# Kernel optimization log

Hardware: AMD Instinct MI355X
Metric: run time of the kernel (lower is better)

## Reference

```python
import jax, jax.numpy as jnp
import numpy as np

B, S, E = 2, 2048, 4096
H, KVH, D = 32, 8, 128
GROUPS = H // KVH
MAX_POS = 4096
ROPE_THETA = 10000.0


def _rope_tables(max_pos, dim, theta):
    inv_freq = 1.0 / (theta ** (jnp.arange(0, dim, 2, dtype=jnp.float32) / dim))
    t = jnp.arange(max_pos, dtype=jnp.float32)
    freqs = jnp.einsum('i,j->ij', t, inv_freq)        # [max_pos, dim/2]
    emb = jnp.concatenate([freqs, freqs], axis=-1)    # [max_pos, dim]
    return jnp.cos(emb), jnp.sin(emb)


def _rotate_half(x):
    x1, x2 = x[..., : x.shape[-1] // 2], x[..., x.shape[-1] // 2:]
    return jnp.concatenate([-x2, x1], axis=-1)


def setup_inputs() -> dict:
    key = jax.random.key(0)
    ks = jax.random.split(key, 8)
    scale_w = 1.0 / np.sqrt(E)
    query = jax.random.normal(ks[0], (B, S, E), dtype=jnp.float32)
    k_in = jax.random.normal(ks[1], (B, S, E), dtype=jnp.float32)
    v_in = jax.random.normal(ks[2], (B, S, E), dtype=jnp.float32)
    position_ids = jnp.broadcast_to(jnp.arange(S, dtype=jnp.int64), (B, S))
    # causal mask: 1 where attending allowed, 0 elsewhere
    src_mask = jnp.tril(jnp.ones((S, S), dtype=jnp.int32))
    src_mask = jnp.broadcast_to(src_mask, (B, S, S))
    Wq = jax.random.normal(ks[3], (E, H * D), dtype=jnp.float32) * scale_w
    Wk = jax.random.normal(ks[4], (E, KVH * D), dtype=jnp.float32) * scale_w
    Wv = jax.random.normal(ks[5], (E, KVH * D), dtype=jnp.float32) * scale_w
    Wo = jax.random.normal(ks[6], (H * D, E), dtype=jnp.float32) * scale_w
    return {"query": query, "key": k_in, "value": v_in,
            "position_ids": position_ids, "src_mask": src_mask,
            "Wq": Wq, "Wk": Wk, "Wv": Wv, "Wo": Wo}


def reference(query, key, value, position_ids, src_mask, Wq, Wk, Wv, Wo):
    nb, q_len, _ = query.shape
    # projections -> [B, heads, S, D]
    q = (query @ Wq).reshape(nb, q_len, H, D).transpose(0, 2, 1, 3)
    k = (key @ Wk).reshape(nb, q_len, KVH, D).transpose(0, 2, 1, 3)
    v = (value @ Wv).reshape(nb, q_len, KVH, D).transpose(0, 2, 1, 3)
    # RoPE
    cos_t, sin_t = _rope_tables(MAX_POS, D, ROPE_THETA)
    cos = cos_t[position_ids][:, None]  # [B,1,S,D]
    sin = sin_t[position_ids][:, None]
    q = q * cos + _rotate_half(q) * sin
    k = k * cos + _rotate_half(k) * sin
    # repeat_kv (interleave groups) -> [B,H,S,D]
    k = jnp.repeat(k, GROUPS, axis=1)
    v = jnp.repeat(v, GROUPS, axis=1)
    # attention core
    scores = jnp.einsum('bhqd,bhkd->bhqk', q, k) / jnp.sqrt(jnp.float32(D))
    mask = src_mask[:, None]  # [B,1,S,S]
    scores = jnp.where(mask == 0, jnp.float32(-1e9), scores)
    attn = jax.nn.softmax(scores, axis=-1)
    x = jnp.einsum('bhqk,bhkd->bhqd', attn, v)
    x = x.transpose(0, 2, 1, 3).reshape(nb, q_len, H * D)
    return x @ Wo
```

## Files before the change

kernel.cpp:

```cpp
#include <hip/hip_runtime.h>
#include <stdint.h>

#define B_ 2
#define S_ 2048
#define E_ 4096
#define H_ 32
#define KVH_ 8
#define D_ 128

typedef __bf16 bf16_t;
typedef __bf16 bf16x8 __attribute__((ext_vector_type(8)));
typedef __bf16 bf16x4 __attribute__((ext_vector_type(4)));
typedef float f32x4 __attribute__((ext_vector_type(4)));

__device__ __forceinline__ void gl2lds16(const void* g, void* l) {
  __builtin_amdgcn_global_load_lds(
      (__attribute__((address_space(1))) void*)(uintptr_t)g,
      (__attribute__((address_space(3))) void*)(uint32_t)(uintptr_t)l,
      16, 0, 0);
}

__global__ void cvt_f32_bf16(const float* __restrict__ in, bf16_t* __restrict__ out, int n4) {
  int i = blockIdx.x * 256 + threadIdx.x;
  if (i < n4) {
    float4 v = ((const float4*)in)[i];
    bf16x4 o;
    o.x = (bf16_t)v.x; o.y = (bf16_t)v.y; o.z = (bf16_t)v.z; o.w = (bf16_t)v.w;
    ((bf16x4*)out)[i] = o;
  }
}

__global__ void transpose_cvt(const float* __restrict__ in, bf16_t* __restrict__ out,
                              int R, int C) {
  __shared__ float t[32][33];
  int r0 = blockIdx.y * 32, c0 = blockIdx.x * 32;
  int tx = threadIdx.x & 31, tg = threadIdx.x >> 5;
#pragma unroll
  for (int k = 0; k < 4; ++k) {
    int r = tg * 4 + k;
    t[r][tx] = in[(long)(r0 + r) * C + c0 + tx];
  }
  __syncthreads();
#pragma unroll
  for (int k = 0; k < 4; ++k) {
    int r = tg * 4 + k;
    out[(long)(c0 + r) * R + r0 + tx] = (bf16_t)t[tx][r];
  }
}

__global__ void transpose_v(const float* __restrict__ Vtmp, bf16_t* __restrict__ Vt) {
  __shared__ float t[32][33];
  int z = blockIdx.z, b = z >> 3, kv = z & 7;
  const float* in = Vtmp + (long)b * S_ * (KVH_ * D_) + kv * D_;
  bf16_t* out = Vt + ((long)(b * KVH_ + kv)) * D_ * S_;
  int s0 = blockIdx.y * 32, d0 = blockIdx.x * 32;
  int tx = threadIdx.x & 31, tg = threadIdx.x >> 5;
#pragma unroll
  for (int k = 0; k < 4; ++k) {
    int r = tg * 4 + k;
    t[r][tx] = in[(long)(s0 + r) * (KVH_ * D_) + d0 + tx];
  }
  __syncthreads();
#pragma unroll
  for (int k = 0; k < 4; ++k) {
    int r = tg * 4 + k;
    out[(long)(d0 + r) * S_ + s0 + tx] = (bf16_t)t[tx][r];
  }
}

__global__ void rope_cvt(const float* __restrict__ T, bf16_t* __restrict__ out,
                         const int* __restrict__ pos, int NH, float scale) {
  long idx = (long)blockIdx.x * 256 + threadIdx.x;
  int j = (int)(idx & 63);
  long t = idx >> 6;
  int s = (int)(t % S_); t /= S_;
  int nh = (int)(t % NH);
  int b = (int)(t / NH);
  long row = ((long)b * S_ + s) * ((long)NH * D_) + (long)nh * D_;
  float x1 = T[row + j];
  float x2 = T[row + j + 64];
  float p = (float)pos[(long)b * S_ + s];
  float inv = expf(-(float)j * (9.210340371976184f / 64.0f));
  float fr = p * inv;
  float c = cosf(fr), sn = sinf(fr);
  long ob = (((long)b * NH + nh) * S_ + s) * D_;
  out[ob + j]      = (bf16_t)((x1 * c - x2 * sn) * scale);
  out[ob + j + 64] = (bf16_t)((x2 * c + x1 * sn) * scale);
}

__global__ __launch_bounds__(256, 2) void gemm_bt(
    const bf16_t* __restrict__ A, const bf16_t* __restrict__ Bt,
    float* __restrict__ C, int M, int N, int K) {
  __shared__ bf16_t As[128 * 64];
  __shared__ bf16_t Bs[128 * 64];
  const int tid = threadIdx.x;
  const int lane = tid & 63;
  const int wave = tid >> 6;
  const int m0 = blockIdx.y * 128, n0 = blockIdx.x * 128;
  const int wm = (wave >> 1) * 64, wn = (wave & 1) * 64;
  const int ln = lane & 15, quad = lane >> 4;
  const int srow = lane >> 3;
  const int sg = lane & 7;

  f32x4 acc[4][4] = {};

  for (int kb = 0; kb < K; kb += 64) {
    __syncthreads();
#pragma unroll
    for (int it = 0; it < 4; ++it) {
      int c = wave * 4 + it;
      int row = c * 8 + srow;
      int g = sg ^ (row & 7);
      gl2lds16(A + (long)(m0 + row) * K + kb + g * 8, &As[c * 512 + lane * 8]);
      gl2lds16(Bt + (long)(n0 + row) * K + kb + g * 8, &Bs[c * 512 + lane * 8]);
    }
    __syncthreads();
#pragma unroll
    for (int ks = 0; ks < 2; ++ks) {
      bf16x8 af[4], bfr[4];
      const int go = ((ks * 4 + quad) ^ (ln & 7)) * 8;
#pragma unroll
      for (int i = 0; i < 4; ++i)
        af[i] = *(const bf16x8*)&As[(wm + i * 16 + ln) * 64 + go];
#pragma unroll
      for (int j = 0; j < 4; ++j)
        bfr[j] = *(const bf16x8*)&Bs[(wn + j * 16 + ln) * 64 + go];
#pragma unroll
      for (int i = 0; i < 4; ++i)
#pragma unroll
        for (int j = 0; j < 4; ++j)
          acc[i][j] = __builtin_amdgcn_mfma_f32_16x16x32_bf16(af[i], bfr[j], acc[i][j], 0, 0, 0);
    }
  }
#pragma unroll
  for (int i = 0; i < 4; ++i)
#pragma unroll
    for (int j = 0; j < 4; ++j)
#pragma unroll
      for (int r = 0; r < 4; ++r) {
        int m = m0 + wm + i * 16 + quad * 4 + r;
        int n = n0 + wn + j * 16 + ln;
        C[(long)m * N + n] = acc[i][j][r];
      }
}

#define QBLK_ 256
#define KVBLK_ 64
__global__ __launch_bounds__(512, 1) void flash_attn(
    const bf16_t* __restrict__ Q, const bf16_t* __restrict__ Kr,
    const bf16_t* __restrict__ Vt, bf16_t* __restrict__ X) {
  __shared__ bf16_t Ks[3][KVBLK_ * D_];
  __shared__ bf16_t Vs[3][D_ * KVBLK_];
  __shared__ bf16_t Plds[8][32 * KVBLK_];
  const int tid = threadIdx.x, lane = tid & 63, wave = tid >> 6;
  const int ln = lane & 15, quad = lane >> 4;

  const int d = blockIdx.x;
  const int wid = (d & 7) * 64 + (d >> 3);
  const int qb = 7 - (wid & 7);
  const int h = (wid >> 3) & 31;
  const int b = wid >> 8;
  const int kv = h >> 2;
  const bf16_t* Kbase = Kr + (((long)b * KVH_ + kv) * S_) * D_;
  const bf16_t* Vbase = Vt + (((long)b * KVH_ + kv) * D_) * S_;
  bf16_t* Pw = Plds[wave];

  const int nt = 4 * qb + 4;
  const int jlast = 4 * qb + (wave >> 1);

  bf16x8 aq[2][4];
  {
    const bf16_t* Qw = Q + (((long)b * H_ + h) * S_ + qb * QBLK_ + wave * 32) * D_;
#pragma unroll
    for (int i = 0; i < 2; ++i)
#pragma unroll
      for (int ks = 0; ks < 4; ++ks)
        aq[i][ks] = *(const bf16x8*)(Qw + (i * 16 + ln) * D_ + ks * 32 + quad * 8);
  }
  asm volatile("s_waitcnt vmcnt(0)" ::: "memory");

  auto STAGE = [&](int bi, int jt) {
    const bf16_t* Kt = Kbase + (long)jt * KVBLK_ * D_;
    const int vcol = jt * KVBLK_;
#pragma unroll
    for (int it = 0; it < 2; ++it) {
      int c = wave * 2 + it;
      int krow = c * 4 + quad;
      int kg = ln ^ (krow & 15);
      gl2lds16(Kt + krow * D_ + kg * 8, &Ks[bi][c * 512 + lane * 8]);
      int vrow = c * 8 + (lane >> 3);
      int vg = (lane & 7) ^ (vrow & 7);
      gl2lds16(Vbase + (long)vrow * S_ + vcol + vg * 8, &Vs[bi][c * 512 + lane * 8]);
    }
  };

  f32x4 o_acc[2][8] = {};
  float m_cur[2][4], l_par[2][4];
#pragma unroll
  for (int i = 0; i < 2; ++i)
#pragma unroll
    for (int r = 0; r < 4; ++r) { m_cur[i][r] = -__builtin_inff(); l_par[i][r] = 0.f; }

  STAGE(0, 0);
  STAGE(1, 1);

  for (int jt = 0; jt < nt; ++jt) {
    if (jt < nt - 1) asm volatile("s_waitcnt vmcnt(4)" ::: "memory");
    else             asm volatile("s_waitcnt vmcnt(0)" ::: "memory");
    __builtin_amdgcn_s_barrier();
    __builtin_amdgcn_sched_barrier(0);
    if (jt + 2 < nt) STAGE((jt + 2) % 3, jt + 2);

    if (jt <= jlast) {
      const bf16_t* Kb = Ks[jt % 3];
      const bf16_t* Vb = Vs[jt % 3];

      f32x4 s_acc[2][4] = {};
#pragma unroll
      for (int ks = 0; ks < 4; ++ks) {
        bf16x8 bk[4];
        const int go = ((ks * 4 + quad) ^ ln) * 8;
#pragma unroll
        for (int j = 0; j < 4; ++j)
          bk[j] = *(const bf16x8*)&Kb[(j * 16 + ln) * D_ + go];
        __builtin_amdgcn_s_setprio(1);
#pragma unroll
        for (int i = 0; i < 2; ++i)
#pragma unroll
          for (int j = 0; j < 4; ++j)
            s_acc[i][j] = __builtin_amdgcn_mfma_f32_16x16x32_bf16(aq[i][ks], bk[j], s_acc[i][j], 0, 0, 0);
        __builtin_amdgcn_s_setprio(0);
      }

#pragma unroll
      for (int i = 0; i < 2; ++i) {
        float rmax[4];
#pragma unroll
        for (int r = 0; r < 4; ++r) rmax[r] = -__builtin_inff();
#pragma unroll
        for (int j = 0; j < 4; ++j)
#pragma unroll
          for (int r = 0; r < 4; ++r) {
            float v = s_acc[i][j][r];
            if (jt == jlast) {
              int qrow = qb * QBLK_ + wave * 32 + i * 16 + quad * 4 + r;
              int kcol = jt * KVBLK_ + j * 16 + ln;
              if (kcol > qrow) v = -__builtin_inff();
            }
            s_acc[i][j][r] = v;
            rmax[r] = fmaxf(rmax[r], v);
          }
#pragma unroll
        for (int r = 0; r < 4; ++r) {
          float v = rmax[r];
          v = fmaxf(v, __shfl_xor(v, 1));
          v = fmaxf(v, __shfl_xor(v, 2));
          v = fmaxf(v, __shfl_xor(v, 4));
          v = fmaxf(v, __shfl_xor(v, 8));
          rmax[r] = v;
        }
        float grow = fmaxf(fmaxf(rmax[0] - m_cur[i][0], rmax[1] - m_cur[i][1]),
                           fmaxf(rmax[2] - m_cur[i][2], rmax[3] - m_cur[i][3]));
        if (__any(grow > 8.0f)) {
          float alpha[4];
#pragma unroll
          for (int r = 0; r < 4; ++r) {
            float mn = fmaxf(m_cur[i][r], rmax[r]);
            alpha[r] = exp2f(m_cur[i][r] - mn);
            m_cur[i][r] = mn;
            l_par[i][r] *= alpha[r];
          }
#pragma unroll
          for (int j = 0; j < 8; ++j)
#pragma unroll
            for (int r = 0; r < 4; ++r)
              o_acc[i][j][r] *= alpha[r];
        }
#pragma unroll
        for (int j = 0; j < 4; ++j)
#pragma unroll
          for (int r = 0; r < 4; ++r) {
            float p = exp2f(s_acc[i][j][r] - m_cur[i][r]);
            s_acc[i][j][r] = p;
            l_par[i][r] += p;
          }
#pragma unroll
        for (int j = 0; j < 4; ++j)
#pragma unroll
          for (int r = 0; r < 4; ++r) {
            int prow = i * 16 + quad * 4 + r;
            int pg = (j * 2 + (ln >> 3)) ^ (prow & 7);
            Pw[prow * KVBLK_ + pg * 8 + (ln & 7)] = (bf16_t)s_acc[i][j][r];
          }
      }

#pragma unroll
      for (int ks = 0; ks < 2; ++ks) {
        bf16x8 ap[2], bv[8];
        const int go = ((ks * 4 + quad) ^ (ln & 7)) * 8;
#pragma unroll
        for (int i = 0; i < 2; ++i)
          ap[i] = *(const bf16x8*)&Pw[(i * 16 + ln) * KVBLK_ + go];
#pragma unroll
        for (int j = 0; j < 8; ++j)
          bv[j] = *(const bf16x8*)&Vb[(j * 16 + ln) * KVBLK_ + go];
        __builtin_amdgcn_s_setprio(1);
#pragma unroll
        for (int i = 0; i < 2; ++i)
#pragma unroll
          for (int j = 0; j < 8; ++j)
            o_acc[i][j] = __builtin_amdgcn_mfma_f32_16x16x32_bf16(ap[i], bv[j], o_acc[i][j], 0, 0, 0);
        __builtin_amdgcn_s_setprio(0);
      }
    }
  }

#pragma unroll
  for (int i = 0; i < 2; ++i) {
    float rl[4];
#pragma unroll
    for (int r = 0; r < 4; ++r) {
      float lsum = l_par[i][r];
      lsum += __shfl_xor(lsum, 1);
      lsum += __shfl_xor(lsum, 2);
      lsum += __shfl_xor(lsum, 4);
      lsum += __shfl_xor(lsum, 8);
      rl[r] = 1.0f / lsum;
    }
#pragma unroll
    for (int j = 0; j < 8; ++j)
#pragma unroll
      for (int r = 0; r < 4; ++r) {
        int q = qb * QBLK_ + wave * 32 + i * 16 + quad * 4 + r;
        int dcol = j * 16 + ln;
        float o = o_acc[i][j][r] * rl[r];
        X[((long)b * S_ + q) * (H_ * D_) + (long)h * D_ + dcol] = (bf16_t)o;
      }
  }
}

extern "C" void kernel_launch(void* const* d_in, const int* in_sizes, int n_in,
                              void* d_out, int out_size, void* d_ws, size_t ws_size,
                              hipStream_t stream) {
  const float* query = (const float*)d_in[0];
  const float* key   = (const float*)d_in[1];
  const float* value = (const float*)d_in[2];
  const int*   pos   = (const int*)d_in[3];
  const float* Wq = (const float*)d_in[5];
  const float* Wk = (const float*)d_in[6];
  const float* Wv = (const float*)d_in[7];
  const float* Wo = (const float*)d_in[8];
  float* out = (float*)d_out;

  char* ws = (char*)d_ws;
  size_t off = 0;
  auto alloc = [&](size_t bytes) {
    char* p = ws + off;
    off += (bytes + 1023) & ~(size_t)1023;
    return p;
  };
  bf16_t* Wqt = (bf16_t*)alloc(33554432);
  bf16_t* Wkt = (bf16_t*)alloc(8388608);
  bf16_t* Wvt = (bf16_t*)alloc(8388608);
  bf16_t* Wot = (bf16_t*)alloc(33554432);
  bf16_t* Xq  = (bf16_t*)alloc(33554432);
  bf16_t* Xk  = (bf16_t*)alloc(33554432);
  bf16_t* Xv  = (bf16_t*)alloc(33554432);
  float*  Ktmp = (float*)alloc(16777216);
  float*  Vtmp = (float*)alloc(16777216);
  float*  Qtmp = out;
  bf16_t* Qr = Xk;
  bf16_t* Kr = Xv;
  bf16_t* Vt = (bf16_t*)((char*)Xv + 8388608);
  bf16_t* X  = Xq;

  const int n4 = B_ * S_ * E_ / 4;
  cvt_f32_bf16<<<n4 / 256, 256, 0, stream>>>(query, Xq, n4);
  cvt_f32_bf16<<<n4 / 256, 256, 0, stream>>>(key, Xk, n4);
  cvt_f32_bf16<<<n4 / 256, 256, 0, stream>>>(value, Xv, n4);

  transpose_cvt<<<dim3(128, 128), 256, 0, stream>>>(Wq, Wqt, 4096, 4096);
  transpose_cvt<<<dim3(32, 128), 256, 0, stream>>>(Wk, Wkt, 4096, 1024);
  transpose_cvt<<<dim3(32, 128), 256, 0, stream>>>(Wv, Wvt, 4096, 1024);
  transpose_cvt<<<dim3(128, 128), 256, 0, stream>>>(Wo, Wot, 4096, 4096);

  gemm_bt<<<dim3(32, 32), 256, 0, stream>>>(Xq, Wqt, Qtmp, 4096, 4096, 4096);
  gemm_bt<<<dim3(8, 32), 256, 0, stream>>>(Xk, Wkt, Ktmp, 4096, 1024, 4096);
  gemm_bt<<<dim3(8, 32), 256, 0, stream>>>(Xv, Wvt, Vtmp, 4096, 1024, 4096);

  rope_cvt<<<(B_ * H_ * S_ * 64) / 256, 256, 0, stream>>>(Qtmp, Qr, pos, H_, 0.12751743f);
  rope_cvt<<<(B_ * KVH_ * S_ * 64) / 256, 256, 0, stream>>>(Ktmp, Kr, pos, KVH_, 1.0f);
  transpose_v<<<dim3(4, 64, 16), 256, 0, stream>>>(Vtmp, Vt);

  flash_attn<<<dim3(512), 512, 0, stream>>>(Qr, Kr, Vt, X);

  gemm_bt<<<dim3(32, 32), 256, 0, stream>>>(X, Wot, out, 4096, 4096, 4096);
}
```

Baseline: 1.116 ms.

## Halve flash-attention Q block, use 4-wave blocks with double buffering and lazy row-max reduction

The Q block shrinks from 256 to 128 rows, so each block has 4 waves instead of 8, and the grid doubles to 1024 blocks. The KV pipeline goes from triple to double buffering, with a full vmcnt(0) wait each iteration. The row-max shuffle reduction now runs only inside the rescale branch; the grow check uses per-lane maxima. This aims to improve load balance and occupancy through smaller blocks and less LDS, at the cost of less K/V reuse per block and more exposed load latency.

```diff
diff --git a/kernel.cpp b/kernel.cpp
--- a/kernel.cpp
+++ b/kernel.cpp
@@ -144,33 +144,33 @@
       }
 }
 
-#define QBLK_ 256
+#define QBLK_ 128
 #define KVBLK_ 64
-__global__ __launch_bounds__(512, 1) void flash_attn(
+__global__ __launch_bounds__(256, 1) void flash_attn(
     const bf16_t* __restrict__ Q, const bf16_t* __restrict__ Kr,
     const bf16_t* __restrict__ Vt, bf16_t* __restrict__ X) {
-  __shared__ bf16_t Ks[3][KVBLK_ * D_];
-  __shared__ bf16_t Vs[3][D_ * KVBLK_];
-  __shared__ bf16_t Plds[8][32 * KVBLK_];
+  __shared__ bf16_t Ks[2][KVBLK_ * D_];
+  __shared__ bf16_t Vs[2][D_ * KVBLK_];
+  __shared__ bf16_t Plds[4][32 * KVBLK_];
   const int tid = threadIdx.x, lane = tid & 63, wave = tid >> 6;
   const int ln = lane & 15, quad = lane >> 4;
 
   const int d = blockIdx.x;
-  const int wid = (d & 7) * 64 + (d >> 3);
-  const int qb = 7 - (wid & 7);
-  const int h = (wid >> 3) & 31;
-  const int b = wid >> 8;
+  const int wid = (d & 7) * 128 + (d >> 3);
+  const int qi = 15 - (wid & 15);
+  const int h = (wid >> 4) & 31;
+  const int b = wid >> 9;
   const int kv = h >> 2;
   const bf16_t* Kbase = Kr + (((long)b * KVH_ + kv) * S_) * D_;
   const bf16_t* Vbase = Vt + (((long)b * KVH_ + kv) * D_) * S_;
   bf16_t* Pw = Plds[wave];
 
-  const int nt = 4 * qb + 4;
-  const int jlast = 4 * qb + (wave >> 1);
+  const int nt = 2 * qi + 2;
+  const int jlast = 2 * qi + (wave >> 1);
 
   bf16x8 aq[2][4];
   {
-    const bf16_t* Qw = Q + (((long)b * H_ + h) * S_ + qb * QBLK_ + wave * 32) * D_;
+    const bf16_t* Qw = Q + (((long)b * H_ + h) * S_ + qi * QBLK_ + wave * 32) * D_;
 #pragma unroll
     for (int i = 0; i < 2; ++i)
 #pragma unroll
@@ -183,8 +183,8 @@
     const bf16_t* Kt = Kbase + (long)jt * KVBLK_ * D_;
     const int vcol = jt * KVBLK_;
 #pragma unroll
-    for (int it = 0; it < 2; ++it) {
-      int c = wave * 2 + it;
+    for (int it = 0; it < 4; ++it) {
+      int c = wave * 4 + it;
       int krow = c * 4 + quad;
       int kg = ln ^ (krow & 15);
       gl2lds16(Kt + krow * D_ + kg * 8, &Ks[bi][c * 512 + lane * 8]);
@@ -202,18 +202,16 @@
     for (int r = 0; r < 4; ++r) { m_cur[i][r] = -__builtin_inff(); l_par[i][r] = 0.f; }
 
   STAGE(0, 0);
-  STAGE(1, 1);
 
   for (int jt = 0; jt < nt; ++jt) {
-    if (jt < nt - 1) asm volatile("s_waitcnt vmcnt(4)" ::: "memory");
-    else             asm volatile("s_waitcnt vmcnt(0)" ::: "memory");
+    asm volatile("s_waitcnt vmcnt(0)" ::: "memory");
     __builtin_amdgcn_s_barrier();
     __builtin_amdgcn_sched_barrier(0);
-    if (jt + 2 < nt) STAGE((jt + 2) % 3, jt + 2);
+    if (jt + 1 < nt) STAGE((jt + 1) & 1, jt + 1);
 
     if (jt <= jlast) {
-      const bf16_t* Kb = Ks[jt % 3];
-      const bf16_t* Vb = Vs[jt % 3];
+      const bf16_t* Kb = Ks[jt & 1];
+      const bf16_t* Vb = Vs[jt & 1];
 
       f32x4 s_acc[2][4] = {};
 #pragma unroll
@@ -234,38 +232,34 @@
 
 #pragma unroll
       for (int i = 0; i < 2; ++i) {
-        float rmax[4];
-#pragma unroll
-        for (int r = 0; r < 4; ++r) rmax[r] = -__builtin_inff();
+        float lmax[4];
+#pragma unroll
+        for (int r = 0; r < 4; ++r) lmax[r] = -__builtin_inff();
 #pragma unroll
         for (int j = 0; j < 4; ++j)
 #pragma unroll
           for (int r = 0; r < 4; ++r) {
             float v = s_acc[i][j][r];
             if (jt == jlast) {
-              int qrow = qb * QBLK_ + wave * 32 + i * 16 + quad * 4 + r;
+              int qrow = qi * QBLK_ + wave * 32 + i * 16 + quad * 4 + r;
               int kcol = jt * KVBLK_ + j * 16 + ln;
               if (kcol > qrow) v = -__builtin_inff();
             }
             s_acc[i][j][r] = v;
-            rmax[r] = fmaxf(rmax[r], v);
+            lmax[r] = fmaxf(lmax[r], v);
           }
-#pragma unroll
-        for (int r = 0; r < 4; ++r) {
-          float v = rmax[r];
-          v = fmaxf(v, __shfl_xor(v, 1));
-          v = fmaxf(v, __shfl_xor(v, 2));
-          v = fmaxf(v, __shfl_xor(v, 4));
-          v = fmaxf(v, __shfl_xor(v, 8));
-          rmax[r] = v;
-        }
-        float grow = fmaxf(fmaxf(rmax[0] - m_cur[i][0], rmax[1] - m_cur[i][1]),
-                           fmaxf(rmax[2] - m_cur[i][2], rmax[3] - m_cur[i][3]));
+        float grow = fmaxf(fmaxf(lmax[0] - m_cur[i][0], lmax[1] - m_cur[i][1]),
+                           fmaxf(lmax[2] - m_cur[i][2], lmax[3] - m_cur[i][3]));
         if (__any(grow > 8.0f)) {
           float alpha[4];
 #pragma unroll
           for (int r = 0; r < 4; ++r) {
-            float mn = fmaxf(m_cur[i][r], rmax[r]);
+            float v = lmax[r];
+            v = fmaxf(v, __shfl_xor(v, 1));
+            v = fmaxf(v, __shfl_xor(v, 2));
+            v = fmaxf(v, __shfl_xor(v, 4));
+            v = fmaxf(v, __shfl_xor(v, 8));
+            float mn = fmaxf(m_cur[i][r], v);
             alpha[r] = exp2f(m_cur[i][r] - mn);
             m_cur[i][r] = mn;
             l_par[i][r] *= alpha[r];
@@ -331,7 +325,7 @@
     for (int j = 0; j < 8; ++j)
 #pragma unroll
       for (int r = 0; r < 4; ++r) {
-        int q = qb * QBLK_ + wave * 32 + i * 16 + quad * 4 + r;
+        int q = qi * QBLK_ + wave * 32 + i * 16 + quad * 4 + r;
         int dcol = j * 16 + ln;
         float o = o_acc[i][j][r] * rl[r];
         X[((long)b * S_ + q) * (H_ * D_) + (long)h * D_ + dcol] = (bf16_t)o;
@@ -392,7 +386,7 @@
   rope_cvt<<<(B_ * KVH_ * S_ * 64) / 256, 256, 0, stream>>>(Ktmp, Kr, pos, KVH_, 1.0f);
   transpose_v<<<dim3(4, 64, 16), 256, 0, stream>>>(Vtmp, Vt);
 
-  flash_attn<<<dim3(512), 512, 0, stream>>>(Qr, Kr, Vt, X);
+  flash_attn<<<dim3(1024), 256, 0, stream>>>(Qr, Kr, Vt, X);
 
   gemm_bt<<<dim3(32, 32), 256, 0, stream>>>(X, Wot, out, 4096, 4096, 4096);
 }
```

Measured after the change: 1.098 ms. About the same (-1.6%).
